# Kernel optimization log

Measured on AMD Instinct MI355X. Metric: run time of the kernel, lower is better.

The kernel has to match this reference:

```python
import jax, jax.numpy as jnp
import numpy as np
from jax import lax

GROUPS = 32
EPS = 1e-5
N_STEPS = 8   # fixed-step stand-in for adaptive implicit_adams
N_CORR = 2    # trapezoidal (Adams-Moulton) corrector iterations


def group_norm(x, gamma, beta):
    B, C, H, W = x.shape
    xg = x.reshape(B, GROUPS, C // GROUPS, H, W)
    mean = xg.mean(axis=(2, 3, 4), keepdims=True)
    var = xg.var(axis=(2, 3, 4), keepdims=True)
    xg = (xg - mean) * lax.rsqrt(var + EPS)
    return xg.reshape(B, C, H, W) * gamma[None, :, None, None] + beta[None, :, None, None]


def batch_norm1d(x, gamma, beta):  # training-mode batch stats, x: [B,C,L]
    mean = x.mean(axis=(0, 2), keepdims=True)
    var = x.var(axis=(0, 2), keepdims=True)
    return (x - mean) * lax.rsqrt(var + EPS) * gamma[None, :, None] + beta[None, :, None]


def conv1d(x, w, b):  # x [B,Cin,L], w [Cout,Cin,3], pad=1
    y = lax.conv_general_dilated(x, w, (1,), [(1, 1)], dimension_numbers=('NCH', 'OIH', 'NCH'))
    return y + b[None, :, None]


def concat_conv2d(t, x, w, b):  # x [B,C,H,W], w [C, C+1, 3,3], pad=1
    tt = jnp.full_like(x[:, :1], t)
    ttx = jnp.concatenate([tt, x], axis=1)
    y = lax.conv_general_dilated(ttx, w, (1, 1), [(1, 1), (1, 1)], dimension_numbers=('NCHW', 'OIHW', 'NCHW'))
    return y + b[None, :, None, None]


def make_odefunc(cw1, cb1, gn1_g, gn1_b, gn2_g, gn2_b, cw2, cb2, gn3_g, gn3_b):
    def f(t, x):
        out = jax.nn.relu(group_norm(x, gn1_g, gn1_b))
        out = concat_conv2d(t, out, cw1, cb1)
        out = jax.nn.elu(group_norm(out, gn2_g, gn2_b))
        out = concat_conv2d(t, out, cw2, cb2)
        return group_norm(out, gn3_g, gn3_b)
    return f


def ode_integrate(f, y0):
    h = 1.0 / N_STEPS

    def step(y, i):
        t = i.astype(y.dtype) * h
        f0 = f(t, y)
        y1 = y + h * f0  # explicit predictor
        for _ in range(N_CORR):  # implicit (trapezoidal AM) corrector
            y1 = y + 0.5 * h * (f0 + f(t + h, y1))
        return y1, None

    yT, _ = lax.scan(step, y0, jnp.arange(N_STEPS))
    return yT


def setup_inputs() -> dict:
    key = jax.random.key(0)
    ks = jax.random.split(key, 8)
    B, L, C = 16, 4096, 256
    inp = {
        'x': jax.random.normal(ks[0], (B, 4, 1, L), dtype=jnp.float32),
        'w1': jax.random.normal(ks[1], (64, 4, 3), dtype=jnp.float32) * 0.1,
        'b1': jnp.zeros((64,), jnp.float32),
        'bn1_g': jnp.ones((64,), jnp.float32), 'bn1_b': jnp.zeros((64,), jnp.float32),
        'w2': jax.random.normal(ks[2], (256, 64, 3), dtype=jnp.float32) * 0.05,
        'b2': jnp.zeros((256,), jnp.float32),
        'bn2_g': jnp.ones((256,), jnp.float32), 'bn2_b': jnp.zeros((256,), jnp.float32),
        'cw1': jax.random.normal(ks[3], (C, C + 1, 3, 3), dtype=jnp.float32) * 0.02,
        'cb1': jnp.zeros((C,), jnp.float32),
        'gn1_g': jnp.ones((C,), jnp.float32), 'gn1_b': jnp.zeros((C,), jnp.float32),
        'gn2_g': jnp.ones((C,), jnp.float32), 'gn2_b': jnp.zeros((C,), jnp.float32),
        'cw2': jax.random.normal(ks[4], (C, C + 1, 3, 3), dtype=jnp.float32) * 0.02,
        'cb2': jnp.zeros((C,), jnp.float32),
        'gn3_g': jnp.ones((C,), jnp.float32), 'gn3_b': jnp.zeros((C,), jnp.float32),
    }
    return inp


def reference(x, w1, b1, bn1_g, bn1_b, w2, b2, bn2_g, bn2_b,
              cw1, cb1, gn1_g, gn1_b, gn2_g, gn2_b, cw2, cb2, gn3_g, gn3_b):
    h = x[:, :, 0, :]                       # squeeze(2) -> [B,4,L]
    h = jax.nn.relu(batch_norm1d(conv1d(h, w1, b1), bn1_g, bn1_b))
    h = jnp.tanh(batch_norm1d(conv1d(h, w2, b2), bn2_g, bn2_b))
    y0 = h[:, :, None, :]                   # unsqueeze(2) -> [B,256,1,L]
    f = make_odefunc(cw1, cb1, gn1_g, gn1_b, gn2_g, gn2_b, cw2, cb2, gn3_g, gn3_b)
    return ode_integrate(f, y0)
```

## Files before the change

kernel.cpp:

```cpp
#include <hip/hip_runtime.h>
#include <math.h>

#define L4 4096

typedef short bf16x8 __attribute__((ext_vector_type(8)));
typedef float f32x4 __attribute__((ext_vector_type(4)));

__device__ __forceinline__ unsigned short f2bf(float f) {
  unsigned u = __builtin_bit_cast(unsigned, f);
  return (unsigned short)((u + 0x7FFFu + ((u >> 16) & 1u)) >> 16);
}
__device__ __forceinline__ float bf2f(unsigned short h) {
  unsigned u = ((unsigned)h) << 16;
  return __builtin_bit_cast(float, u);
}
__device__ __forceinline__ unsigned pk2(float lo, float hi) {
  unsigned d;
  asm("v_cvt_pk_bf16_f32 %0, %1, %2" : "=v"(d) : "v"(lo), "v"(hi));
  return d;
}
__device__ __forceinline__ float fast_tanh(float x) {
  float e = __expf(2.f * x);
  return 1.f - 2.f * __builtin_amdgcn_rcpf(e + 1.f);
}

__global__ __launch_bounds__(256) void pack_big(const float* __restrict__ cw,
                                                unsigned short* __restrict__ Apack,
                                                float* __restrict__ Tpack) {
  int gid = blockIdx.x * 256 + threadIdx.x;
  if (gid < 768) {
    int o = gid & 255, tap = gid >> 8;
    Tpack[tap * 256 + o] = cw[((size_t)o * 257) * 9 + 3 + tap];
  }
  if (gid >= 24 * 16 * 64) return;
  int ks = gid >> 10;
  int frow = (gid >> 6) & 15;
  int lane = gid & 63;
  int o = frow * 16 + (lane & 15);
  int tap = ks >> 3;
  int ib = ((ks & 7) << 5) + ((lane >> 4) << 3);
#pragma unroll
  for (int e = 0; e < 8; e++) {
    int i = ib + e;
    Apack[(size_t)gid * 8 + e] = f2bf(cw[((size_t)o * 257 + (i + 1)) * 9 + 3 + tap]);
  }
}

__global__ __launch_bounds__(256) void pack_stem(const float* __restrict__ w2,
                                                 unsigned short* __restrict__ Apack) {
  int gid = blockIdx.x * 256 + threadIdx.x;
  if (gid >= 6 * 16 * 64) return;
  int ks = gid >> 10;
  int frow = (gid >> 6) & 15;
  int lane = gid & 63;
  int o = frow * 16 + (lane & 15);
  int tap = ks >> 1;
  int ib = ((ks & 1) << 5) + ((lane >> 4) << 3);
#pragma unroll
  for (int e = 0; e < 8; e++) {
    int i = ib + e;
    Apack[(size_t)gid * 8 + e] = f2bf(w2[((size_t)o * 64 + i) * 3 + tap]);
  }
}

__global__ __launch_bounds__(256) void conv1_kernel(const float* __restrict__ x,
                                                    const float* __restrict__ w,
                                                    const float* __restrict__ bias,
                                                    unsigned short* __restrict__ out) {
  int idx = blockIdx.x * 256 + threadIdx.x;
  int l = idx & 4095;
  int c = (idx >> 12) & 63;
  int b = idx >> 18;
  const float* xb = x + (size_t)b * 4 * L4;
  const float* wc = w + c * 12;
  float acc = bias[c];
#pragma unroll
  for (int i = 0; i < 4; i++) {
    float x0 = (l > 0) ? xb[i * L4 + l - 1] : 0.f;
    float x1 = xb[i * L4 + l];
    float x2 = (l < 4095) ? xb[i * L4 + l + 1] : 0.f;
    acc += wc[i * 3] * x0 + wc[i * 3 + 1] * x1 + wc[i * 3 + 2] * x2;
  }
  out[idx] = f2bf(acc);
}

__global__ __launch_bounds__(256) void stats_kernel(const float* __restrict__ in,
                                                    float* __restrict__ stats,
                                                    int unit_stride, int nrow,
                                                    int row_stride, int rowlen,
                                                    float inv_n) {
  int u = blockIdx.x;
  const float* base = in + (size_t)u * unit_stride;
  float s = 0.f, s2 = 0.f;
  for (int r = 0; r < nrow; r++) {
    const float* rowp = base + (size_t)r * row_stride;
    for (int j = threadIdx.x * 4; j < rowlen; j += 256 * 4) {
      float4 v = *(const float4*)(rowp + j);
      s += v.x + v.y + v.z + v.w;
      s2 += v.x * v.x + v.y * v.y + v.z * v.z + v.w * v.w;
    }
  }
  __shared__ float sh[512];
  sh[threadIdx.x] = s;
  sh[256 + threadIdx.x] = s2;
  __syncthreads();
  for (int off = 128; off > 0; off >>= 1) {
    if (threadIdx.x < off) {
      sh[threadIdx.x] += sh[threadIdx.x + off];
      sh[256 + threadIdx.x] += sh[256 + threadIdx.x + off];
    }
    __syncthreads();
  }
  if (threadIdx.x == 0) {
    float m = sh[0] * inv_n;
    float var = sh[256] * inv_n - m * m;
    stats[u * 2] = m;
    stats[u * 2 + 1] = rsqrtf(var + 1e-5f);
  }
}

__global__ __launch_bounds__(256) void stats_bf16_kernel(const unsigned short* __restrict__ in,
                                                         float* __restrict__ stats,
                                                         int unit_stride, int nrow,
                                                         int row_stride, int rowlen,
                                                         float inv_n) {
  int u = blockIdx.x;
  const unsigned short* base = in + (size_t)u * unit_stride;
  float s = 0.f, s2 = 0.f;
  for (int r = 0; r < nrow; r++) {
    const unsigned short* rowp = base + (size_t)r * row_stride;
    for (int j = threadIdx.x * 4; j < rowlen; j += 256 * 4) {
      ushort4 v = *(const ushort4*)(rowp + j);
      float va = bf2f(v.x), vb = bf2f(v.y), vc = bf2f(v.z), vd = bf2f(v.w);
      s += va + vb + vc + vd;
      s2 += va * va + vb * vb + vc * vc + vd * vd;
    }
  }
  __shared__ float sh[512];
  sh[threadIdx.x] = s;
  sh[256 + threadIdx.x] = s2;
  __syncthreads();
  for (int off = 128; off > 0; off >>= 1) {
    if (threadIdx.x < off) {
      sh[threadIdx.x] += sh[threadIdx.x + off];
      sh[256 + threadIdx.x] += sh[256 + threadIdx.x + off];
    }
    __syncthreads();
  }
  if (threadIdx.x == 0) {
    float m = sh[0] * inv_n;
    float var = sh[256] * inv_n - m * m;
    stats[u * 2] = m;
    stats[u * 2 + 1] = rsqrtf(var + 1e-5f);
  }
}

__global__ __launch_bounds__(256) void act_transpose64(const unsigned short* __restrict__ inv,
                                                       const float* __restrict__ stats,
                                                       const float* __restrict__ gamma,
                                                       const float* __restrict__ beta,
                                                       unsigned short* __restrict__ Xt) {
  constexpr int C = 64;
  __shared__ unsigned short tile[64 * C];
  int bidx = blockIdx.x;
  int b = bidx >> 6;
  int lt = bidx & 63;
  int l0 = lt << 6;
  int t = threadIdx.x;
  int lanel = t & 63;
  int cq = t >> 6;
  for (int cp = 0; cp < C / 4; cp++) {
    int c = cp * 4 + cq;
    float m = stats[2 * c], rs = stats[2 * c + 1];
    float ga = gamma[c] * rs, be = beta[c] - m * ga;
    size_t gidx = ((size_t)b * C + c) * 4096 + l0 + lanel;
    float v = bf2f(inv[gidx]);
    float a = v * ga + be;
    float r = fmaxf(a, 0.f);
    int sw = (lanel & 15) << 2;
    tile[lanel * C + (c ^ sw)] = f2bf(r);
  }
  __syncthreads();
  constexpr int CH = C / 4;
  constexpr int RPP = 256 / CH;
  for (int p = 0; p < 64 / RPP; p++) {
    int r = p * RPP + t / CH;
    int ch = t % CH;
    int sw = (r & 15) << 2;
    ushort4 v = *(const ushort4*)&tile[r * C + ((ch * 4) ^ sw)];
    *(ushort4*)&Xt[((size_t)b * 4098 + 1 + l0 + r) * C + ch * 4] = v;
  }
  if (lt == 0) {
    if (t < C / 4) *(ushort4*)&Xt[((size_t)b * 4098 + 0) * C + t * 4] = make_ushort4(0, 0, 0, 0);
  } else if (lt == 63) {
    if (t < C / 4) *(ushort4*)&Xt[((size_t)b * 4098 + 4097) * C + t * 4] = make_ushort4(0, 0, 0, 0);
  }
}

template <int NKS, int KLG, int CIN, int NORM, int ACT, int NCH, bool INBF, bool TCH, int OUT>
__global__ __launch_bounds__(512, 4) void gemm_T(const void* __restrict__ Bsrc,
                                                 const unsigned short* __restrict__ Apack,
                                                 const float* __restrict__ Pin,
                                                 const float* __restrict__ gng,
                                                 const float* __restrict__ gnb,
                                                 const float* __restrict__ Tpack,
                                                 const float* __restrict__ bias,
                                                 float tval,
                                                 void* __restrict__ outv,
                                                 float* __restrict__ Pout) {
  constexpr int CPR = CIN / 8;
  constexpr int CPRLG = (CIN == 256) ? 5 : 3;
  constexpr int ROWS = 66;
  constexpr int RPI = 512 >> CPRLG;
  constexpr int TOT = ROWS * CPR;
  __shared__ unsigned short bsm[ROWS * CIN];
  __shared__ float gsm[32][2];
  __shared__ float ebias[256];
  __shared__ float psh[32][2];

  int tid = threadIdx.x;
  int lane = tid & 63;
  int wv = tid >> 6;
  int b = blockIdx.x >> 6;
  int lt = blockIdx.x & 63;
  int l_base = lt << 6;
  int wo0 = wv << 5;
  int col = lane & 15;
  int grp = lane >> 4;

  if (NORM) {
    int g = tid >> 4, j0 = tid & 15;
    const float* Pg = Pin + ((size_t)b * 32 + g) * 128;
    float s = 0.f, s2 = 0.f;
    for (int j = j0; j < NCH; j += 16) { s += Pg[j * 2]; s2 += Pg[j * 2 + 1]; }
#pragma unroll
    for (int off = 8; off; off >>= 1) { s += __shfl_down(s, off, 16); s2 += __shfl_down(s2, off, 16); }
    if (j0 == 0) {
      float m = s * (1.f / 32768.f);
      float var = s2 * (1.f / 32768.f) - m * m;
      gsm[g][0] = m;
      gsm[g][1] = rsqrtf(var + 1e-5f);
    }
  }
  if (tid < 256) {
    float e = bias[tid];
    if (TCH) e += tval * (Tpack[tid] + Tpack[256 + tid] + Tpack[512 + tid]);
    ebias[tid] = e;
  }
  if (OUT == 0 && tid >= 256 && tid < 288) { psh[tid - 256][0] = 0.f; psh[tid - 256][1] = 0.f; }
  __syncthreads();

  {
    int pl = tid & (CPR - 1);
    int row0 = tid >> CPRLG;
    int gch = pl ^ (row0 & 7);
    float ga0 = 1.f, ga1 = 1.f, ga2 = 1.f, ga3 = 1.f, ga4 = 1.f, ga5 = 1.f, ga6 = 1.f, ga7 = 1.f;
    float be0 = 0.f, be1 = 0.f, be2 = 0.f, be3 = 0.f, be4 = 0.f, be5 = 0.f, be6 = 0.f, be7 = 0.f;
    if (NORM) {
      float m = gsm[gch][0], rs = gsm[gch][1];
      float4 g0 = *(const float4*)&gng[gch * 8];
      float4 g1 = *(const float4*)&gng[gch * 8 + 4];
      float4 b0 = *(const float4*)&gnb[gch * 8];
      float4 b1 = *(const float4*)&gnb[gch * 8 + 4];
      ga0 = g0.x * rs; ga1 = g0.y * rs; ga2 = g0.z * rs; ga3 = g0.w * rs;
      ga4 = g1.x * rs; ga5 = g1.y * rs; ga6 = g1.z * rs; ga7 = g1.w * rs;
      be0 = b0.x - m * ga0; be1 = b0.y - m * ga1; be2 = b0.z - m * ga2; be3 = b0.w - m * ga3;
      be4 = b1.x - m * ga4; be5 = b1.y - m * ga5; be6 = b1.z - m * ga6; be7 = b1.w - m * ga7;
    }
#define ACTF(a) ((ACT == 0) ? fmaxf((a), 0.f) : ((a) > 0.f ? (a) : __expf(a) - 1.f))
#pragma unroll
    for (int it = 0; it < (TOT + 511) / 512; it++) {
      int chunk = it * 512 + tid;
      if (chunk < TOT) {
        int row = row0 + it * RPI;
        uint4 w4;
        if (NORM) {
          int gl = l_base - 1 + row;
          if (gl >= 0 && gl < 4096) {
            size_t base = ((size_t)b * 4096 + gl) * CIN + gch * 8;
            float v0, v1, v2, v3, v4, v5, v6, v7;
            if (INBF) {
              uint4 raw = *(const uint4*)((const unsigned short*)Bsrc + base);
              v0 = bf2f((unsigned short)(raw.x & 0xFFFF)); v1 = bf2f((unsigned short)(raw.x >> 16));
              v2 = bf2f((unsigned short)(raw.y & 0xFFFF)); v3 = bf2f((unsigned short)(raw.y >> 16));
              v4 = bf2f((unsigned short)(raw.z & 0xFFFF)); v5 = bf2f((unsigned short)(raw.z >> 16));
              v6 = bf2f((unsigned short)(raw.w & 0xFFFF)); v7 = bf2f((unsigned short)(raw.w >> 16));
            } else {
              float4 r0 = *(const float4*)((const float*)Bsrc + base);
              float4 r1 = *(const float4*)((const float*)Bsrc + base + 4);
              v0 = r0.x; v1 = r0.y; v2 = r0.z; v3 = r0.w;
              v4 = r1.x; v5 = r1.y; v6 = r1.z; v7 = r1.w;
            }
            float r0 = ACTF(v0 * ga0 + be0), r1 = ACTF(v1 * ga1 + be1);
            float r2 = ACTF(v2 * ga2 + be2), r3 = ACTF(v3 * ga3 + be3);
            float r4 = ACTF(v4 * ga4 + be4), r5 = ACTF(v5 * ga5 + be5);
            float r6 = ACTF(v6 * ga6 + be6), r7 = ACTF(v7 * ga7 + be7);
            w4.x = pk2(r0, r1); w4.y = pk2(r2, r3);
            w4.z = pk2(r4, r5); w4.w = pk2(r6, r7);
          } else {
            w4 = make_uint4(0, 0, 0, 0);
          }
        } else {
          w4 = *(const uint4*)((const unsigned short*)Bsrc +
                               ((size_t)b * 4098 + l_base + row) * CIN + gch * 8);
        }
        *(uint4*)&bsm[(size_t)chunk * 8] = w4;
      }
    }
#undef ACTF
  }
  __syncthreads();

  const unsigned short* apk = Apack + (size_t)(wv * 2) * 512 + (size_t)lane * 8;

  f32x4 acc[2][4];
#pragma unroll
  for (int i = 0; i < 2; i++)
#pragma unroll
    for (int j = 0; j < 4; j++) acc[i][j] = (f32x4){0.f, 0.f, 0.f, 0.f};

#pragma unroll
  for (int ksp = 0; ksp < NKS; ksp += 2) {
    const unsigned short* apA = apk + (size_t)ksp * 16 * 512;
    const unsigned short* apB = apk + (size_t)(ksp + 1) * 16 * 512;
    bf16x8 a00 = *(const bf16x8*)(apA);
    bf16x8 a01 = *(const bf16x8*)(apA + 512);
    bf16x8 a10 = *(const bf16x8*)(apB);
    bf16x8 a11 = *(const bf16x8*)(apB + 512);
    {
      int ks = ksp;
      int tap = ks >> KLG;
      int cbase = (ks & ((1 << KLG) - 1)) << 2;
      int lr0 = col + tap;
      int cb = (cbase + grp) ^ (lr0 & 7);
      const unsigned short* bp = &bsm[((size_t)(lr0 << CPRLG) + cb) * 8];
      bf16x8 bfr[4];
#pragma unroll
      for (int fc = 0; fc < 4; fc++) bfr[fc] = *(const bf16x8*)(bp + fc * 16 * CIN);
#pragma unroll
      for (int fc = 0; fc < 4; fc++) {
        acc[0][fc] = __builtin_amdgcn_mfma_f32_16x16x32_bf16(a00, bfr[fc], acc[0][fc], 0, 0, 0);
        acc[1][fc] = __builtin_amdgcn_mfma_f32_16x16x32_bf16(a01, bfr[fc], acc[1][fc], 0, 0, 0);
      }
    }
    {
      int ks = ksp + 1;
      int tap = ks >> KLG;
      int cbase = (ks & ((1 << KLG) - 1)) << 2;
      int lr0 = col + tap;
      int cb = (cbase + grp) ^ (lr0 & 7);
      const unsigned short* bp = &bsm[((size_t)(lr0 << CPRLG) + cb) * 8];
      bf16x8 bfr[4];
#pragma unroll
      for (int fc = 0; fc < 4; fc++) bfr[fc] = *(const bf16x8*)(bp + fc * 16 * CIN);
#pragma unroll
      for (int fc = 0; fc < 4; fc++) {
        acc[0][fc] = __builtin_amdgcn_mfma_f32_16x16x32_bf16(a10, bfr[fc], acc[0][fc], 0, 0, 0);
        acc[1][fc] = __builtin_amdgcn_mfma_f32_16x16x32_bf16(a11, bfr[fc], acc[1][fc], 0, 0, 0);
      }
    }
  }

  float ps = 0.f, ps2 = 0.f;
#pragma unroll
  for (int fo = 0; fo < 2; fo++) {
    int o0 = wo0 + fo * 16 + grp * 4;
    float eb0 = ebias[o0], eb1 = ebias[o0 + 1], eb2 = ebias[o0 + 2], eb3 = ebias[o0 + 3];
    float w0c0 = 0.f, w0c1 = 0.f, w0c2 = 0.f, w0c3 = 0.f;
    float w2c0 = 0.f, w2c1 = 0.f, w2c2 = 0.f, w2c3 = 0.f;
    if (TCH && lt == 0) {
      w0c0 = tval * Tpack[o0]; w0c1 = tval * Tpack[o0 + 1];
      w0c2 = tval * Tpack[o0 + 2]; w0c3 = tval * Tpack[o0 + 3];
    }
    if (TCH && lt == 63) {
      w2c0 = tval * Tpack[512 + o0]; w2c1 = tval * Tpack[512 + o0 + 1];
      w2c2 = tval * Tpack[512 + o0 + 2]; w2c3 = tval * Tpack[512 + o0 + 3];
    }
#pragma unroll
    for (int fc = 0; fc < 4; fc++) {
      int l = l_base + fc * 16 + col;
      float v0 = acc[fo][fc][0] + eb0;
      float v1 = acc[fo][fc][1] + eb1;
      float v2 = acc[fo][fc][2] + eb2;
      float v3 = acc[fo][fc][3] + eb3;
      if (TCH) {
        if (lt == 0 && l == 0) { v0 -= w0c0; v1 -= w0c1; v2 -= w0c2; v3 -= w0c3; }
        if (lt == 63 && l == 4095) { v0 -= w2c0; v1 -= w2c1; v2 -= w2c2; v3 -= w2c3; }
      }
      if (OUT == 0) {
        ps += v0 + v1 + v2 + v3;
        ps2 += v0 * v0 + v1 * v1 + v2 * v2 + v3 * v3;
        uint2 pk = make_uint2(pk2(v0, v1), pk2(v2, v3));
        *(uint2*)((unsigned short*)outv + ((size_t)b * 4096 + l) * 256 + o0) = pk;
      } else {
        float* op = (float*)outv + ((size_t)b * 256 + o0) * 4096 + l;
        op[0] = v0; op[4096] = v1; op[8192] = v2; op[12288] = v3;
      }
    }
    if (OUT == 0) {
      float s = ps, s2 = ps2;
#pragma unroll
      for (int off = 8; off; off >>= 1) {
        s += __shfl_down(s, off, 16);
        s2 += __shfl_down(s2, off, 16);
      }
      if (col == 0) {
        int g = wv * 4 + fo * 2 + (grp >> 1);
        atomicAdd(&psh[g][0], s);
        atomicAdd(&psh[g][1], s2);
      }
      ps = 0.f; ps2 = 0.f;
    }
  }

  if (OUT == 0) {
    __syncthreads();
    if (tid < 32) {
      size_t pi = ((size_t)b * 32 + tid) * 128 + (size_t)lt * 2;
      Pout[pi] = psh[tid][0];
      Pout[pi + 1] = psh[tid][1];
    }
  }
}

__global__ __launch_bounds__(512) void bn_tanh_T(const float* __restrict__ Q,
                                                 const float* __restrict__ stats,
                                                 const float* __restrict__ gamma,
                                                 const float* __restrict__ beta,
                                                 float* __restrict__ Y,
                                                 float* __restrict__ P1) {
  int tid = threadIdx.x;
  int b = blockIdx.x >> 5;
  int seg = blockIdx.x & 31;
  int c = tid >> 1;
  float m = stats[2 * c], rs = stats[2 * c + 1];
  float ga = gamma[c] * rs, be = beta[c] - m * ga;
  __shared__ float psh[32][2];
  if (tid < 32) { psh[tid][0] = 0.f; psh[tid][1] = 0.f; }
  __syncthreads();
  float s = 0.f, s2 = 0.f;
  for (int it = 0; it < 16; it++) {
    int l4 = (tid & 1) + it * 2;
    int l0 = seg * 128 + l4 * 4;
    float4 v = *(const float4*)&Q[((size_t)b * 256 + c) * 4096 + l0];
    float r0 = fast_tanh(v.x * ga + be);
    float r1 = fast_tanh(v.y * ga + be);
    float r2 = fast_tanh(v.z * ga + be);
    float r3 = fast_tanh(v.w * ga + be);
    Y[((size_t)b * 4096 + l0 + 0) * 256 + c] = r0;
    Y[((size_t)b * 4096 + l0 + 1) * 256 + c] = r1;
    Y[((size_t)b * 4096 + l0 + 2) * 256 + c] = r2;
    Y[((size_t)b * 4096 + l0 + 3) * 256 + c] = r3;
    s += r0 + r1 + r2 + r3;
    s2 += r0 * r0 + r1 * r1 + r2 * r2 + r3 * r3;
  }
#pragma unroll
  for (int off = 8; off; off >>= 1) { s += __shfl_down(s, off, 16); s2 += __shfl_down(s2, off, 16); }
  if ((tid & 15) == 0) {
    int g = c >> 3;
    atomicAdd(&psh[g][0], s);
    atomicAdd(&psh[g][1], s2);
  }
  __syncthreads();
  if (tid < 32) {
    size_t pi = ((size_t)b * 32 + tid) * 128 + (size_t)seg * 2;
    P1[pi] = psh[tid][0];
    P1[pi + 1] = psh[tid][1];
  }
}

template <int MODE>
__global__ __launch_bounds__(512) void combine_T(const unsigned short* __restrict__ F,
                                                 const float* __restrict__ P3,
                                                 const float* __restrict__ gng,
                                                 const float* __restrict__ gnb,
                                                 float* __restrict__ Y,
                                                 unsigned short* __restrict__ Y1,
                                                 float* __restrict__ P1) {
  __shared__ float gsm[32][2];
  __shared__ float gabe[256][2];
  __shared__ float psh[32][2];
  int tid = threadIdx.x;
  int b = blockIdx.x >> 5;
  int seg = blockIdx.x & 31;
  {
    int g = tid >> 4, j0 = tid & 15;
    const float* Pg = P3 + ((size_t)b * 32 + g) * 128;
    float s = 0.f, s2 = 0.f;
    for (int j = j0; j < 64; j += 16) { s += Pg[j * 2]; s2 += Pg[j * 2 + 1]; }
#pragma unroll
    for (int off = 8; off; off >>= 1) { s += __shfl_down(s, off, 16); s2 += __shfl_down(s2, off, 16); }
    if (j0 == 0) {
      float m = s * (1.f / 32768.f);
      float var = s2 * (1.f / 32768.f) - m * m;
      gsm[g][0] = m;
      gsm[g][1] = rsqrtf(var + 1e-5f);
    }
  }
  __syncthreads();
  if (tid < 256) {
    float m = gsm[tid >> 3][0], rs = gsm[tid >> 3][1];
    float ga = gng[tid] * rs;
    gabe[tid][0] = ga;
    gabe[tid][1] = gnb[tid] - m * ga;
  }
  if (tid >= 256 && tid < 288) { psh[tid - 256][0] = 0.f; psh[tid - 256][1] = 0.f; }
  __syncthreads();

  size_t base4 = ((size_t)b * 4096 + seg * 128) * 64;
  int c0 = (tid << 2) & 255;
  int g = c0 >> 3;
  float ga0 = gabe[c0][0], be0 = gabe[c0][1];
  float ga1 = gabe[c0 + 1][0], be1 = gabe[c0 + 1][1];
  float ga2 = gabe[c0 + 2][0], be2 = gabe[c0 + 2][1];
  float ga3 = gabe[c0 + 3][0], be3 = gabe[c0 + 3][1];
  float s = 0.f, s2 = 0.f;
  for (int i = tid; i < 8192; i += 512) {
    size_t idx4 = base4 + i;
    ushort4 fv = ((const ushort4*)F)[idx4];
    float4 yv = ((const float4*)Y)[idx4];
    float f0 = bf2f(fv.x) * ga0 + be0;
    float f1 = bf2f(fv.y) * ga1 + be1;
    float f2 = bf2f(fv.z) * ga2 + be2;
    float f3 = bf2f(fv.w) * ga3 + be3;
    float4 yn;
    yn.x = yv.x + (MODE == 0 ? 0.125f : 0.0625f) * f0;
    yn.y = yv.y + (MODE == 0 ? 0.125f : 0.0625f) * f1;
    yn.z = yv.z + (MODE == 0 ? 0.125f : 0.0625f) * f2;
    yn.w = yv.w + (MODE == 0 ? 0.125f : 0.0625f) * f3;
    if (MODE == 0) {
      float4 yb;
      yb.x = yv.x + 0.0625f * f0;
      yb.y = yv.y + 0.0625f * f1;
      yb.z = yv.z + 0.0625f * f2;
      yb.w = yv.w + 0.0625f * f3;
      ((float4*)Y)[idx4] = yb;
    }
    if (MODE == 2) {
      ((float4*)Y)[idx4] = yn;
    } else {
      uint2 pk = make_uint2(pk2(yn.x, yn.y), pk2(yn.z, yn.w));
      ((uint2*)Y1)[idx4] = pk;
    }
    s += yn.x + yn.y + yn.z + yn.w;
    s2 += yn.x * yn.x + yn.y * yn.y + yn.z * yn.z + yn.w * yn.w;
  }
  s += __shfl_xor(s, 1);
  s2 += __shfl_xor(s2, 1);
  if ((tid & 1) == 0) {
    atomicAdd(&psh[g][0], s);
    atomicAdd(&psh[g][1], s2);
  }
  __syncthreads();
  if (tid < 32) {
    size_t pi = ((size_t)b * 32 + tid) * 128 + (size_t)seg * 2;
    P1[pi] = psh[tid][0];
    P1[pi + 1] = psh[tid][1];
  }
}

__global__ __launch_bounds__(256) void transpose_final(const float* __restrict__ Y,
                                                       float* __restrict__ out) {
  __shared__ float tile[64 * 260];
  int b = blockIdx.x >> 6;
  int lt = blockIdx.x & 63;
  int t = threadIdx.x;
  for (int i = t; i < 4096; i += 256) {
    int r = i >> 6;
    int c4 = (i & 63) << 2;
    float4 v = *(const float4*)&Y[((size_t)b * 4096 + lt * 64 + r) * 256 + c4];
    *(float4*)&tile[r * 260 + c4] = v;
  }
  __syncthreads();
  for (int i = t; i < 4096; i += 256) {
    int c = i >> 4;
    int l4 = (i & 15) << 2;
    float4 v;
    v.x = tile[(l4 + 0) * 260 + c];
    v.y = tile[(l4 + 1) * 260 + c];
    v.z = tile[(l4 + 2) * 260 + c];
    v.w = tile[(l4 + 3) * 260 + c];
    *(float4*)&out[((size_t)b * 256 + c) * 4096 + lt * 64 + l4] = v;
  }
}

extern "C" void kernel_launch(void* const* d_in, const int* in_sizes, int n_in,
                              void* d_out, int out_size, void* d_ws, size_t ws_size,
                              hipStream_t stream) {
  const float* x = (const float*)d_in[0];
  const float* w1 = (const float*)d_in[1];
  const float* b1 = (const float*)d_in[2];
  const float* bn1_g = (const float*)d_in[3];
  const float* bn1_b = (const float*)d_in[4];
  const float* w2 = (const float*)d_in[5];
  const float* b2 = (const float*)d_in[6];
  const float* bn2_g = (const float*)d_in[7];
  const float* bn2_b = (const float*)d_in[8];
  const float* cw1 = (const float*)d_in[9];
  const float* cb1 = (const float*)d_in[10];
  const float* gn1_g = (const float*)d_in[11];
  const float* gn1_b = (const float*)d_in[12];
  const float* gn2_g = (const float*)d_in[13];
  const float* gn2_b = (const float*)d_in[14];
  const float* cw2 = (const float*)d_in[15];
  const float* cb2 = (const float*)d_in[16];
  const float* gn3_g = (const float*)d_in[17];
  const float* gn3_b = (const float*)d_in[18];

  const size_t SZ = (size_t)16 * 256 * 4096;

  char* p = (char*)d_ws;
  float* Ybuf = (float*)p;                   p += SZ * 4;
  unsigned short* C1 = (unsigned short*)p;   p += SZ * 2;
  unsigned short* Fb = (unsigned short*)p;   p += SZ * 2;
  unsigned short* APK1 = (unsigned short*)p; p += (size_t)24 * 16 * 64 * 8 * 2;
  unsigned short* APK2 = (unsigned short*)p; p += (size_t)24 * 16 * 64 * 8 * 2;
  unsigned short* APKS = (unsigned short*)p; p += (size_t)6 * 16 * 64 * 8 * 2;
  float* TP1 = (float*)p;                    p += 768 * 4;
  float* TP2 = (float*)p;                    p += 768 * 4;
  float* STATS = (float*)p;                  p += 1024 * 4;
  float* P1 = (float*)p;                     p += (size_t)16 * 32 * 128 * 4;
  float* P2 = (float*)p;                     p += (size_t)16 * 32 * 128 * 4;
  float* P3 = (float*)p;                     p += (size_t)16 * 32 * 128 * 4;

  float* Q = (float*)d_out;
  unsigned short* Y1 = (unsigned short*)d_out;

  pack_big<<<96, 256, 0, stream>>>(cw1, APK1, TP1);
  pack_big<<<96, 256, 0, stream>>>(cw2, APK2, TP2);
  pack_stem<<<24, 256, 0, stream>>>(w2, APKS);

  conv1_kernel<<<16384, 256, 0, stream>>>(x, w1, b1, C1);
  stats_bf16_kernel<<<64, 256, 0, stream>>>(C1, STATS, 4096, 16, 64 * 4096, 4096, 1.f / 65536.f);
  act_transpose64<<<1024, 256, 0, stream>>>(C1, STATS, bn1_g, bn1_b, Fb);
  gemm_T<6, 1, 64, 0, 0, 32, true, false, 1><<<1024, 512, 0, stream>>>(
      Fb, APKS, nullptr, nullptr, nullptr, nullptr, b2, 0.f, Q, nullptr);
  stats_kernel<<<256, 256, 0, stream>>>(Q, STATS, 4096, 16, 256 * 4096, 4096, 1.f / 65536.f);
  bn_tanh_T<<<512, 512, 0, stream>>>(Q, STATS, bn2_g, bn2_b, Ybuf, P1);

  const float H = 0.125f;
  for (int i = 0; i < 8; i++) {
    float t = i * H;
    gemm_T<24, 3, 256, 1, 0, 32, false, true, 0><<<1024, 512, 0, stream>>>(
        Ybuf, APK1, P1, gn1_g, gn1_b, TP1, cb1, t, C1, P2);
    gemm_T<24, 3, 256, 1, 1, 64, true, true, 0><<<1024, 512, 0, stream>>>(
        C1, APK2, P2, gn2_g, gn2_b, TP2, cb2, t, Fb, P3);
    combine_T<0><<<512, 512, 0, stream>>>(Fb, P3, gn3_g, gn3_b, Ybuf, Y1, P1);
    for (int c = 0; c < 2; c++) {
      gemm_T<24, 3, 256, 1, 0, 32, true, true, 0><<<1024, 512, 0, stream>>>(
          Y1, APK1, P1, gn1_g, gn1_b, TP1, cb1, t + H, C1, P2);
      gemm_T<24, 3, 256, 1, 1, 64, true, true, 0><<<1024, 512, 0, stream>>>(
          C1, APK2, P2, gn2_g, gn2_b, TP2, cb2, t + H, Fb, P3);
      if (c == 0)
        combine_T<1><<<512, 512, 0, stream>>>(Fb, P3, gn3_g, gn3_b, Ybuf, Y1, P1);
      else
        combine_T<2><<<512, 512, 0, stream>>>(Fb, P3, gn3_g, gn3_b, Ybuf, Y1, P1);
    }
  }

  transpose_final<<<1024, 256, 0, stream>>>(Ybuf, (float*)d_out);
}
```

Measured before the change: 2.682 ms.

## Store ODE state in bf16 and prefetch A fragments in GEMM loop

The ODE state buffer changes from fp32 to bf16 throughout: the tanh stem output, the combine kernels (which now read bf16 state and write bf16 predictor/base buffers, with the base buffer placed in the second half of the output buffer), the first conv GEMM input, and the final transpose. This halves state memory traffic in the combine and GEMM loads, but each step accumulates in bf16, which risks precision drift across the 24 steps. Separately, the GEMM inner loop software-prefetches the next A-fragment pair into registers and raises wave priority during the MFMA loop. The prefetch hides load latency at the cost of extra registers.

```diff
diff --git a/kernel.cpp b/kernel.cpp
--- a/kernel.cpp
+++ b/kernel.cpp
@@ -319,14 +319,24 @@
 #pragma unroll
     for (int j = 0; j < 4; j++) acc[i][j] = (f32x4){0.f, 0.f, 0.f, 0.f};
 
+  __builtin_amdgcn_s_setprio(1);
+  bf16x8 a00 = *(const bf16x8*)(apk);
+  bf16x8 a01 = *(const bf16x8*)(apk + 512);
+  bf16x8 a10 = *(const bf16x8*)(apk + 8192);
+  bf16x8 a11 = *(const bf16x8*)(apk + 8192 + 512);
 #pragma unroll
   for (int ksp = 0; ksp < NKS; ksp += 2) {
-    const unsigned short* apA = apk + (size_t)ksp * 16 * 512;
-    const unsigned short* apB = apk + (size_t)(ksp + 1) * 16 * 512;
-    bf16x8 a00 = *(const bf16x8*)(apA);
-    bf16x8 a01 = *(const bf16x8*)(apA + 512);
-    bf16x8 a10 = *(const bf16x8*)(apB);
-    bf16x8 a11 = *(const bf16x8*)(apB + 512);
+    bf16x8 n00, n01, n10, n11;
+    constexpr bool dummy = false; (void)dummy;
+    bool more = (ksp + 2) < NKS;
+    if (more) {
+      const unsigned short* apN0 = apk + (size_t)(ksp + 2) * 8192;
+      const unsigned short* apN1 = apk + (size_t)(ksp + 3) * 8192;
+      n00 = *(const bf16x8*)(apN0);
+      n01 = *(const bf16x8*)(apN0 + 512);
+      n10 = *(const bf16x8*)(apN1);
+      n11 = *(const bf16x8*)(apN1 + 512);
+    }
     {
       int ks = ksp;
       int tap = ks >> KLG;
@@ -359,7 +369,9 @@
         acc[1][fc] = __builtin_amdgcn_mfma_f32_16x16x32_bf16(a11, bfr[fc], acc[1][fc], 0, 0, 0);
       }
     }
-  }
+    if (more) { a00 = n00; a01 = n01; a10 = n10; a11 = n11; }
+  }
+  __builtin_amdgcn_s_setprio(0);
 
   float ps = 0.f, ps2 = 0.f;
 #pragma unroll
@@ -427,7 +439,7 @@
                                                  const float* __restrict__ stats,
                                                  const float* __restrict__ gamma,
                                                  const float* __restrict__ beta,
-                                                 float* __restrict__ Y,
+                                                 unsigned short* __restrict__ Y,
                                                  float* __restrict__ P1) {
   int tid = threadIdx.x;
   int b = blockIdx.x >> 5;
@@ -447,10 +459,10 @@
     float r1 = fast_tanh(v.y * ga + be);
     float r2 = fast_tanh(v.z * ga + be);
     float r3 = fast_tanh(v.w * ga + be);
-    Y[((size_t)b * 4096 + l0 + 0) * 256 + c] = r0;
-    Y[((size_t)b * 4096 + l0 + 1) * 256 + c] = r1;
-    Y[((size_t)b * 4096 + l0 + 2) * 256 + c] = r2;
-    Y[((size_t)b * 4096 + l0 + 3) * 256 + c] = r3;
+    Y[((size_t)b * 4096 + l0 + 0) * 256 + c] = f2bf(r0);
+    Y[((size_t)b * 4096 + l0 + 1) * 256 + c] = f2bf(r1);
+    Y[((size_t)b * 4096 + l0 + 2) * 256 + c] = f2bf(r2);
+    Y[((size_t)b * 4096 + l0 + 3) * 256 + c] = f2bf(r3);
     s += r0 + r1 + r2 + r3;
     s2 += r0 * r0 + r1 * r1 + r2 * r2 + r3 * r3;
   }
@@ -474,8 +486,9 @@
                                                  const float* __restrict__ P3,
                                                  const float* __restrict__ gng,
                                                  const float* __restrict__ gnb,
-                                                 float* __restrict__ Y,
-                                                 unsigned short* __restrict__ Y1,
+                                                 const unsigned short* __restrict__ Yin,
+                                                 unsigned short* __restrict__ Out1,
+                                                 unsigned short* __restrict__ OutB,
                                                  float* __restrict__ P1) {
   __shared__ float gsm[32][2];
   __shared__ float gabe[256][2];
@@ -518,32 +531,26 @@
   for (int i = tid; i < 8192; i += 512) {
     size_t idx4 = base4 + i;
     ushort4 fv = ((const ushort4*)F)[idx4];
-    float4 yv = ((const float4*)Y)[idx4];
+    ushort4 yv = ((const ushort4*)Yin)[idx4];
+    float y0 = bf2f(yv.x), y1v = bf2f(yv.y), y2 = bf2f(yv.z), y3 = bf2f(yv.w);
     float f0 = bf2f(fv.x) * ga0 + be0;
     float f1 = bf2f(fv.y) * ga1 + be1;
     float f2 = bf2f(fv.z) * ga2 + be2;
     float f3 = bf2f(fv.w) * ga3 + be3;
-    float4 yn;
-    yn.x = yv.x + (MODE == 0 ? 0.125f : 0.0625f) * f0;
-    yn.y = yv.y + (MODE == 0 ? 0.125f : 0.0625f) * f1;
-    yn.z = yv.z + (MODE == 0 ? 0.125f : 0.0625f) * f2;
-    yn.w = yv.w + (MODE == 0 ? 0.125f : 0.0625f) * f3;
+    float yn0 = y0 + (MODE == 0 ? 0.125f : 0.0625f) * f0;
+    float yn1 = y1v + (MODE == 0 ? 0.125f : 0.0625f) * f1;
+    float yn2 = y2 + (MODE == 0 ? 0.125f : 0.0625f) * f2;
+    float yn3 = y3 + (MODE == 0 ? 0.125f : 0.0625f) * f3;
+    ((uint2*)Out1)[idx4] = make_uint2(pk2(yn0, yn1), pk2(yn2, yn3));
     if (MODE == 0) {
-      float4 yb;
-      yb.x = yv.x + 0.0625f * f0;
-      yb.y = yv.y + 0.0625f * f1;
-      yb.z = yv.z + 0.0625f * f2;
-      yb.w = yv.w + 0.0625f * f3;
-      ((float4*)Y)[idx4] = yb;
-    }
-    if (MODE == 2) {
-      ((float4*)Y)[idx4] = yn;
-    } else {
-      uint2 pk = make_uint2(pk2(yn.x, yn.y), pk2(yn.z, yn.w));
-      ((uint2*)Y1)[idx4] = pk;
-    }
-    s += yn.x + yn.y + yn.z + yn.w;
-    s2 += yn.x * yn.x + yn.y * yn.y + yn.z * yn.z + yn.w * yn.w;
+      float yb0 = y0 + 0.0625f * f0;
+      float yb1 = y1v + 0.0625f * f1;
+      float yb2 = y2 + 0.0625f * f2;
+      float yb3 = y3 + 0.0625f * f3;
+      ((uint2*)OutB)[idx4] = make_uint2(pk2(yb0, yb1), pk2(yb2, yb3));
+    }
+    s += yn0 + yn1 + yn2 + yn3;
+    s2 += yn0 * yn0 + yn1 * yn1 + yn2 * yn2 + yn3 * yn3;
   }
   s += __shfl_xor(s, 1);
   s2 += __shfl_xor(s2, 1);
@@ -559,27 +566,27 @@
   }
 }
 
-__global__ __launch_bounds__(256) void transpose_final(const float* __restrict__ Y,
+__global__ __launch_bounds__(256) void transpose_final(const unsigned short* __restrict__ Y,
                                                        float* __restrict__ out) {
-  __shared__ float tile[64 * 260];
+  __shared__ unsigned short tile[64 * 260];
   int b = blockIdx.x >> 6;
   int lt = blockIdx.x & 63;
   int t = threadIdx.x;
   for (int i = t; i < 4096; i += 256) {
     int r = i >> 6;
     int c4 = (i & 63) << 2;
-    float4 v = *(const float4*)&Y[((size_t)b * 4096 + lt * 64 + r) * 256 + c4];
-    *(float4*)&tile[r * 260 + c4] = v;
+    ushort4 v = *(const ushort4*)&Y[((size_t)b * 4096 + lt * 64 + r) * 256 + c4];
+    *(ushort4*)&tile[r * 260 + c4] = v;
   }
   __syncthreads();
   for (int i = t; i < 4096; i += 256) {
     int c = i >> 4;
     int l4 = (i & 15) << 2;
     float4 v;
-    v.x = tile[(l4 + 0) * 260 + c];
-    v.y = tile[(l4 + 1) * 260 + c];
-    v.z = tile[(l4 + 2) * 260 + c];
-    v.w = tile[(l4 + 3) * 260 + c];
+    v.x = bf2f(tile[(l4 + 0) * 260 + c]);
+    v.y = bf2f(tile[(l4 + 1) * 260 + c]);
+    v.z = bf2f(tile[(l4 + 2) * 260 + c]);
+    v.w = bf2f(tile[(l4 + 3) * 260 + c]);
     *(float4*)&out[((size_t)b * 256 + c) * 4096 + lt * 64 + l4] = v;
   }
 }
@@ -610,7 +617,7 @@
   const size_t SZ = (size_t)16 * 256 * 4096;
 
   char* p = (char*)d_ws;
-  float* Ybuf = (float*)p;                   p += SZ * 4;
+  unsigned short* Ybf = (unsigned short*)p;  p += SZ * 2;
   unsigned short* C1 = (unsigned short*)p;   p += SZ * 2;
   unsigned short* Fb = (unsigned short*)p;   p += SZ * 2;
   unsigned short* APK1 = (unsigned short*)p; p += (size_t)24 * 16 * 64 * 8 * 2;
@@ -625,6 +632,7 @@
 
   float* Q = (float*)d_out;
   unsigned short* Y1 = (unsigned short*)d_out;
+  unsigned short* YB = Y1 + SZ;
 
   pack_big<<<96, 256, 0, stream>>>(cw1, APK1, TP1);
   pack_big<<<96, 256, 0, stream>>>(cw2, APK2, TP2);
@@ -636,27 +644,27 @@
   gemm_T<6, 1, 64, 0, 0, 32, true, false, 1><<<1024, 512, 0, stream>>>(
       Fb, APKS, nullptr, nullptr, nullptr, nullptr, b2, 0.f, Q, nullptr);
   stats_kernel<<<256, 256, 0, stream>>>(Q, STATS, 4096, 16, 256 * 4096, 4096, 1.f / 65536.f);
-  bn_tanh_T<<<512, 512, 0, stream>>>(Q, STATS, bn2_g, bn2_b, Ybuf, P1);
+  bn_tanh_T<<<512, 512, 0, stream>>>(Q, STATS, bn2_g, bn2_b, Ybf, P1);
 
   const float H = 0.125f;
   for (int i = 0; i < 8; i++) {
     float t = i * H;
-    gemm_T<24, 3, 256, 1, 0, 32, false, true, 0><<<1024, 512, 0, stream>>>(
-        Ybuf, APK1, P1, gn1_g, gn1_b, TP1, cb1, t, C1, P2);
+    gemm_T<24, 3, 256, 1, 0, 32, true, true, 0><<<1024, 512, 0, stream>>>(
+        Ybf, APK1, P1, gn1_g, gn1_b, TP1, cb1, t, C1, P2);
     gemm_T<24, 3, 256, 1, 1, 64, true, true, 0><<<1024, 512, 0, stream>>>(
         C1, APK2, P2, gn2_g, gn2_b, TP2, cb2, t, Fb, P3);
-    combine_T<0><<<512, 512, 0, stream>>>(Fb, P3, gn3_g, gn3_b, Ybuf, Y1, P1);
+    combine_T<0><<<512, 512, 0, stream>>>(Fb, P3, gn3_g, gn3_b, Ybf, Y1, YB, P1);
     for (int c = 0; c < 2; c++) {
       gemm_T<24, 3, 256, 1, 0, 32, true, true, 0><<<1024, 512, 0, stream>>>(
           Y1, APK1, P1, gn1_g, gn1_b, TP1, cb1, t + H, C1, P2);
       gemm_T<24, 3, 256, 1, 1, 64, true, true, 0><<<1024, 512, 0, stream>>>(
           C1, APK2, P2, gn2_g, gn2_b, TP2, cb2, t + H, Fb, P3);
       if (c == 0)
-        combine_T<1><<<512, 512, 0, stream>>>(Fb, P3, gn3_g, gn3_b, Ybuf, Y1, P1);
+        combine_T<1><<<512, 512, 0, stream>>>(Fb, P3, gn3_g, gn3_b, YB, Y1, nullptr, P1);
       else
-        combine_T<2><<<512, 512, 0, stream>>>(Fb, P3, gn3_g, gn3_b, Ybuf, Y1, P1);
-    }
-  }
-
-  transpose_final<<<1024, 256, 0, stream>>>(Ybuf, (float*)d_out);
-}
+        combine_T<2><<<512, 512, 0, stream>>>(Fb, P3, gn3_g, gn3_b, YB, Ybf, nullptr, P1);
+    }
+  }
+
+  transpose_final<<<1024, 256, 0, stream>>>(Ybf, (float*)d_out);
+}
```

New measurement: 2.420 ms. 1.11x faster.
